# Kernel optimization log

Measured on AMD Instinct MI355X. Metric: run time of the kernel, lower is better.

The kernel has to match this reference:

```python
import jax, jax.numpy as jnp
import numpy as np

B, L, D, H = 2, 2048, 1024, 16
HD = D // H
SCALE = 1.0 / (HD ** 0.5)


def setup_inputs() -> dict:
    key = jax.random.key(0)
    ks = jax.random.split(key, 8)
    s = 0.02  # keep pre-softmax logits in a sane range
    return {
        "x": jax.random.normal(ks[0], (B, L, D), dtype=jnp.float32),
        "attn_biases": jax.random.normal(ks[1], (B, H, L, L), dtype=jnp.float32) * 0.1,
        "attn_mask": jnp.zeros((B, 1, L, L), dtype=jnp.float32),
        "Wq": jax.random.normal(ks[2], (D, D), dtype=jnp.float32) * s,
        "bq": jnp.zeros((D,), dtype=jnp.float32),
        "Wk": jax.random.normal(ks[3], (D, D), dtype=jnp.float32) * s,
        "bk": jnp.zeros((D,), dtype=jnp.float32),
        "Wv": jax.random.normal(ks[4], (D, D), dtype=jnp.float32) * s,
        "bv": jnp.zeros((D,), dtype=jnp.float32),
        "Wo": jax.random.normal(ks[5], (D, D), dtype=jnp.float32) * s,
        "bo": jnp.zeros((D,), dtype=jnp.float32),
    }


def reference(x, attn_biases, attn_mask, Wq, bq, Wk, bk, Wv, bv, Wo, bo):
    b, l, d = x.shape
    # torch nn.Linear: y = x @ W.T + b
    q = (x @ Wq.T + bq).reshape(b, l, H, HD)
    k = (x @ Wk.T + bk).reshape(b, l, H, HD)
    v = (x @ Wv.T + bv).reshape(b, l, H, HD)
    # scores: (B, H, Lq, Lk)
    scores = SCALE * jnp.einsum("bqhd,bkhd->bhqk", q, k)
    scores = scores + attn_biases + attn_mask
    probs = jax.nn.softmax(scores, axis=-1)
    out = jnp.einsum("bhqk,bkhd->bqhd", probs, v).reshape(b, l, d)
    return out @ Wo.T + bo
```

## Files before the change

### kernel.cpp

```cpp
#include <hip/hip_runtime.h>
#include <stdint.h>

#define SCALE_ 0.125f

typedef unsigned short u16;
typedef __attribute__((ext_vector_type(8))) __bf16 bf16x8;
typedef __attribute__((ext_vector_type(4))) float f32x4;
typedef __attribute__((ext_vector_type(4))) unsigned int u32x4;

__device__ __forceinline__ void gload16(const void* g, void* l) {
  __builtin_amdgcn_global_load_lds(
      (const __attribute__((address_space(1))) unsigned int*)g,
      (__attribute__((address_space(3))) unsigned int*)l, 16, 0, 0);
}

__device__ __forceinline__ u16 f2bf(float f) {
  union { float f; unsigned int u; } v; v.f = f;
  return (u16)((v.u + 0x7FFFu + ((v.u >> 16) & 1u)) >> 16);
}

__device__ __forceinline__ bf16x8 ld_bf8(const u16* p) {
  return *reinterpret_cast<const bf16x8*>(p);
}

__global__ __launch_bounds__(256) void cvt_kernel(
    const float* __restrict__ x, const float* __restrict__ wq,
    const float* __restrict__ wk, const float* __restrict__ wv,
    const float* __restrict__ wo, u16* __restrict__ ws) {
  long e0 = ((long)blockIdx.x * 256 + threadIdx.x) * 8;
  const float* src; u16* dst; long off;
  if (e0 < 4194304L) {
    src = x; dst = ws; off = e0;
  } else {
    long tt = e0 - 4194304L;
    int w = (int)(tt >> 20);
    off = tt & 1048575L;
    src = (w == 0) ? wq : (w == 1) ? wk : (w == 2) ? wv : wo;
    dst = ws + 4194304L + (long)w * 1048576L;
  }
  float4 f0 = *(const float4*)(src + off);
  float4 f1 = *(const float4*)(src + off + 4);
  union { u16 u[8]; u32x4 v; } r;
  r.u[0] = f2bf(f0.x); r.u[1] = f2bf(f0.y); r.u[2] = f2bf(f0.z); r.u[3] = f2bf(f0.w);
  r.u[4] = f2bf(f1.x); r.u[5] = f2bf(f1.y); r.u[6] = f2bf(f1.z); r.u[7] = f2bf(f1.w);
  *reinterpret_cast<u32x4*>(dst + off) = r.v;
}

__global__ __launch_bounds__(256) void gemm_bt(
    const u16* __restrict__ A,
    const u16* __restrict__ W0, const u16* __restrict__ W1, const u16* __restrict__ W2,
    const float* __restrict__ b0, const float* __restrict__ b1, const float* __restrict__ b2,
    void* __restrict__ d0, void* __restrict__ d1, void* __restrict__ d2,
    int mode_base) {
  __shared__ u16 lsA[128 * 32];
  __shared__ u16 lsB[128 * 32];

  const int z = blockIdx.z;
  const int mode = mode_base + z;
  const u16* W = (z == 0) ? W0 : (z == 1) ? W1 : W2;
  const float* bias = (z == 0) ? b0 : (z == 1) ? b1 : b2;
  void* dst = (z == 0) ? d0 : (z == 1) ? d1 : d2;
  const float scale = (mode == 0) ? SCALE_ : 1.0f;

  const int t = threadIdx.x;
  const int bm = blockIdx.y, bn = blockIdx.x;
  const int lane = t & 63, lr = lane & 15, lg = lane >> 4;
  const int wid = t >> 6, wr = wid >> 1, wc = wid & 1;

  f32x4 zero = {0.f, 0.f, 0.f, 0.f};
  f32x4 acc[4][4];
#pragma unroll
  for (int i = 0; i < 4; ++i)
#pragma unroll
    for (int j = 0; j < 4; ++j) acc[i][j] = zero;

  const u16* gA = A + (size_t)(bm * 128) * 1024;
  const u16* gB = W + (size_t)(bn * 128) * 1024;
  const int srow = t >> 2, scol = (t & 3) * 8;

  for (int kt = 0; kt < 32; ++kt) {
    const int k0 = kt * 32;
    __syncthreads();
    gload16(gA + (size_t)srow * 1024 + k0 + scol,        &lsA[t * 8]);
    gload16(gA + (size_t)(srow + 64) * 1024 + k0 + scol, &lsA[2048 + t * 8]);
    gload16(gB + (size_t)srow * 1024 + k0 + scol,        &lsB[t * 8]);
    gload16(gB + (size_t)(srow + 64) * 1024 + k0 + scol, &lsB[2048 + t * 8]);
    __syncthreads();

    bf16x8 af[4], bf[4];
#pragma unroll
    for (int mi = 0; mi < 4; ++mi)
      af[mi] = ld_bf8(&lsA[(wr * 64 + mi * 16 + lr) * 32 + lg * 8]);
#pragma unroll
    for (int ni = 0; ni < 4; ++ni)
      bf[ni] = ld_bf8(&lsB[(wc * 64 + ni * 16 + lr) * 32 + lg * 8]);
#pragma unroll
    for (int mi = 0; mi < 4; ++mi)
#pragma unroll
      for (int ni = 0; ni < 4; ++ni)
        acc[mi][ni] = __builtin_amdgcn_mfma_f32_16x16x32_bf16(af[mi], bf[ni], acc[mi][ni], 0, 0, 0);
  }

#pragma unroll
  for (int ni = 0; ni < 4; ++ni) {
    const int gcol = bn * 128 + wc * 64 + ni * 16 + lr;
    const float bv = bias[gcol];
#pragma unroll
    for (int mi = 0; mi < 4; ++mi) {
      const int growb = bm * 128 + wr * 64 + mi * 16 + lg * 4;
#pragma unroll
      for (int j = 0; j < 4; ++j) {
        const int grow = growb + j;
        const float val = (acc[mi][ni][j] + bv) * scale;
        if (mode == 3) {
          ((float*)dst)[(size_t)grow * 1024 + gcol] = val;
        } else {
          const int b = grow >> 11, l = grow & 2047, h = gcol >> 6, hd = gcol & 63;
          size_t idx;
          if (mode == 2) idx = (((size_t)(b * 16 + h)) * 64 + hd) * 2048 + l;
          else           idx = (((size_t)(b * 16 + h)) * 2048 + l) * 64 + hd;
          ((u16*)dst)[idx] = f2bf(val);
        }
      }
    }
  }
}

__global__ __launch_bounds__(256) void gemm_out64(
    const u16* __restrict__ A, const u16* __restrict__ W,
    const float* __restrict__ bias, float* __restrict__ out) {
  __shared__ u16 lsA[64 * 32];
  __shared__ u16 lsB[128 * 32];

  const int t = threadIdx.x;
  const int bm = blockIdx.y, bn = blockIdx.x;
  const int lane = t & 63, lr = lane & 15, lg = lane >> 4;
  const int wid = t >> 6;

  f32x4 zero = {0.f, 0.f, 0.f, 0.f};
  f32x4 acc[4][2];
#pragma unroll
  for (int i = 0; i < 4; ++i) { acc[i][0] = zero; acc[i][1] = zero; }

  const u16* gA = A + (size_t)(bm * 64) * 1024;
  const u16* gB = W + (size_t)(bn * 128) * 1024;
  const int srow = t >> 2, scol = (t & 3) * 8;

  for (int kt = 0; kt < 32; ++kt) {
    const int k0 = kt * 32;
    __syncthreads();
    gload16(gA + (size_t)srow * 1024 + k0 + scol,        &lsA[t * 8]);
    gload16(gB + (size_t)srow * 1024 + k0 + scol,        &lsB[t * 8]);
    gload16(gB + (size_t)(srow + 64) * 1024 + k0 + scol, &lsB[2048 + t * 8]);
    __syncthreads();

    bf16x8 af[4], bf[2];
#pragma unroll
    for (int mi = 0; mi < 4; ++mi)
      af[mi] = ld_bf8(&lsA[(mi * 16 + lr) * 32 + lg * 8]);
#pragma unroll
    for (int ni = 0; ni < 2; ++ni)
      bf[ni] = ld_bf8(&lsB[(wid * 32 + ni * 16 + lr) * 32 + lg * 8]);
#pragma unroll
    for (int mi = 0; mi < 4; ++mi)
#pragma unroll
      for (int ni = 0; ni < 2; ++ni)
        acc[mi][ni] = __builtin_amdgcn_mfma_f32_16x16x32_bf16(af[mi], bf[ni], acc[mi][ni], 0, 0, 0);
  }

#pragma unroll
  for (int ni = 0; ni < 2; ++ni) {
    const int gcol = bn * 128 + wid * 32 + ni * 16 + lr;
    const float bv = bias[gcol];
#pragma unroll
    for (int mi = 0; mi < 4; ++mi) {
      const int growb = bm * 64 + mi * 16 + lg * 4;
#pragma unroll
      for (int j = 0; j < 4; ++j)
        out[(size_t)(growb + j) * 1024 + gcol] = acc[mi][ni][j] + bv;
    }
  }
}

__global__ __launch_bounds__(256, 4) void attn_kernel(
    const u16* __restrict__ Q, const u16* __restrict__ Kb_, const u16* __restrict__ Vtb,
    const float* __restrict__ bias, const float* __restrict__ mask,
    u16* __restrict__ attn) {
  __shared__ u16 lsK[64 * 64];
  __shared__ u16 lsV[64 * 64];
  __shared__ u16 lsP[4][16 * 88];

  const int t = threadIdx.x, wid = t >> 6, lane = t & 63, lr = lane & 15, lg = lane >> 4;
  const int q0 = blockIdx.x * 64;
  const int h = blockIdx.y, b = blockIdx.z;
  const int bh = b * 16 + h;

  const u16* qb = Q + ((size_t)bh * 2048 + q0 + wid * 16) * 64;
  const u16* kb = Kb_ + (size_t)bh * 2048 * 64;
  const u16* vb = Vtb + (size_t)bh * 64 * 2048;
  const float* biasr = bias + (size_t)bh * 2048 * 2048;
  const float* maskr = mask + (size_t)b * 2048 * 2048;

  bf16x8 qf[2];
  qf[0] = ld_bf8(qb + (size_t)lr * 64 + lg * 8);
  qf[1] = ld_bf8(qb + (size_t)lr * 64 + 32 + lg * 8);

  float lsum[4] = {0.f, 0.f, 0.f, 0.f};
  f32x4 zero = {0.f, 0.f, 0.f, 0.f};
  f32x4 o[4];
#pragma unroll
  for (int i = 0; i < 4; ++i) o[i] = zero;

  const int srow = t >> 3;
  const int swz = ((t & 7) ^ (srow & 7)) * 8;
  const int rsw = (lr & 7) * 8;
  const int qrow0 = q0 + wid * 16 + lg * 4;

  for (int kt = 0; kt < 32; ++kt) {
    const int k0 = kt * 64;

    float bb[4][4];
#pragma unroll
    for (int j = 0; j < 4; ++j) {
      const float* br = biasr + (size_t)(qrow0 + j) * 2048 + k0 + lr;
      const float* mr = maskr + (size_t)(qrow0 + j) * 2048 + k0 + lr;
#pragma unroll
      for (int n = 0; n < 4; ++n) bb[j][n] = br[n * 16] + mr[n * 16];
    }

    __syncthreads();
    gload16(kb + (size_t)(k0 + srow) * 64 + swz,        &lsK[t * 8]);
    gload16(kb + (size_t)(k0 + srow + 32) * 64 + swz,   &lsK[2048 + t * 8]);
    gload16(vb + (size_t)srow * 2048 + k0 + swz,        &lsV[t * 8]);
    gload16(vb + (size_t)(srow + 32) * 2048 + k0 + swz, &lsV[2048 + t * 8]);
    __syncthreads();

    f32x4 s[4];
#pragma unroll
    for (int n = 0; n < 4; ++n) s[n] = zero;
#pragma unroll
    for (int ks = 0; ks < 2; ++ks)
#pragma unroll
      for (int n = 0; n < 4; ++n) {
        bf16x8 kf = ld_bf8(&lsK[((n * 16 + lr) * 64 + ks * 32 + lg * 8) ^ rsw]);
        s[n] = __builtin_amdgcn_mfma_f32_16x16x32_bf16(qf[ks], kf, s[n], 0, 0, 0);
      }

#pragma unroll
    for (int i = 0; i < 4; ++i) {
      float rs = 0.f;
#pragma unroll
      for (int n = 0; n < 4; ++n) {
        float p = __expf(s[n][i] + bb[i][n]);
        s[n][i] = p;
        rs += p;
      }
      lsum[i] += rs;
    }

#pragma unroll
    for (int n = 0; n < 4; ++n)
#pragma unroll
      for (int i = 0; i < 4; ++i)
        lsP[wid][(lg * 4 + i) * 88 + n * 16 + lr] = f2bf(s[n][i]);
    asm volatile("s_waitcnt lgkmcnt(0)" ::: "memory");
    __builtin_amdgcn_sched_barrier(0);

#pragma unroll
    for (int ks = 0; ks < 2; ++ks) {
      bf16x8 pa = ld_bf8(&lsP[wid][lr * 88 + ks * 32 + lg * 8]);
#pragma unroll
      for (int dt = 0; dt < 4; ++dt) {
        bf16x8 vf = ld_bf8(&lsV[((dt * 16 + lr) * 64 + ks * 32 + lg * 8) ^ rsw]);
        o[dt] = __builtin_amdgcn_mfma_f32_16x16x32_bf16(pa, vf, o[dt], 0, 0, 0);
      }
    }
  }

#pragma unroll
  for (int i = 0; i < 4; ++i) {
    lsum[i] += __shfl_xor(lsum[i], 1);
    lsum[i] += __shfl_xor(lsum[i], 2);
    lsum[i] += __shfl_xor(lsum[i], 4);
    lsum[i] += __shfl_xor(lsum[i], 8);
  }
  float inv[4];
#pragma unroll
  for (int i = 0; i < 4; ++i) inv[i] = 1.0f / lsum[i];
#pragma unroll
  for (int dt = 0; dt < 4; ++dt) {
    const int dcol = h * 64 + dt * 16 + lr;
#pragma unroll
    for (int i = 0; i < 4; ++i)
      attn[((size_t)b * 2048 + qrow0 + i) * 1024 + dcol] = f2bf(o[dt][i] * inv[i]);
  }
}

extern "C" void kernel_launch(void* const* d_in, const int* in_sizes, int n_in,
                              void* d_out, int out_size, void* d_ws, size_t ws_size,
                              hipStream_t stream) {
  const float* x    = (const float*)d_in[0];
  const float* bias = (const float*)d_in[1];
  const float* mask = (const float*)d_in[2];
  const float* Wq   = (const float*)d_in[3];
  const float* bq   = (const float*)d_in[4];
  const float* Wk   = (const float*)d_in[5];
  const float* bk   = (const float*)d_in[6];
  const float* Wv   = (const float*)d_in[7];
  const float* bv   = (const float*)d_in[8];
  const float* Wo   = (const float*)d_in[9];
  const float* bo   = (const float*)d_in[10];
  float* out = (float*)d_out;

  u16* ws   = (u16*)d_ws;
  u16* xb   = ws;
  u16* wqb  = ws + 4194304L;
  u16* wkb  = wqb + 1048576L;
  u16* wvb  = wkb + 1048576L;
  u16* wob  = wvb + 1048576L;
  u16* Qb   = wob + 1048576L;
  u16* Kb   = Qb + 4194304L;
  u16* Vtb  = Kb + 4194304L;
  u16* attnb = Vtb + 4194304L;

  cvt_kernel<<<4096, 256, 0, stream>>>(x, Wq, Wk, Wv, Wo, ws);

  dim3 gqkv(8, 32, 3);
  gemm_bt<<<gqkv, 256, 0, stream>>>(xb, wqb, wkb, wvb, bq, bk, bv,
                                    (void*)Qb, (void*)Kb, (void*)Vtb, 0);

  attn_kernel<<<dim3(32, 16, 2), 256, 0, stream>>>(Qb, Kb, Vtb, bias, mask, attnb);

  gemm_out64<<<dim3(8, 64), 256, 0, stream>>>(attnb, wob, bo, out);
}
```

Baseline: 241.3 us.

## Double-buffer K/V tiles, prefetch bias, and use exp2 with 512-thread attention blocks

The attention kernel now runs 512 threads per block covering 128 query rows, so each K/V tile in LDS is shared by eight waves. K/V tiles are double-buffered, with the next tile's loads issued before the current tile's compute, which leaves one barrier per iteration. The next tile's bias and mask are loaded after QK^T. Q is pre-scaled by scale·log2e and bias is multiplied by log2e, so softmax uses exp2 and the bias seeds the MFMA accumulator. LDS use per block roughly doubles, and occupancy under launch_bounds(512,4) may change.

```diff
diff --git a/kernel.cpp b/kernel.cpp
--- a/kernel.cpp
+++ b/kernel.cpp
@@ -1,7 +1,8 @@
 #include <hip/hip_runtime.h>
 #include <stdint.h>
 
-#define SCALE_ 0.125f
+#define QSCALE_ 0.18033688f
+#define LOG2E_  1.44269504f
 
 typedef unsigned short u16;
 typedef __attribute__((ext_vector_type(8))) __bf16 bf16x8;
@@ -60,7 +61,7 @@
   const u16* W = (z == 0) ? W0 : (z == 1) ? W1 : W2;
   const float* bias = (z == 0) ? b0 : (z == 1) ? b1 : b2;
   void* dst = (z == 0) ? d0 : (z == 1) ? d1 : d2;
-  const float scale = (mode == 0) ? SCALE_ : 1.0f;
+  const float scale = (mode == 0) ? QSCALE_ : 1.0f;
 
   const int t = threadIdx.x;
   const int bm = blockIdx.y, bn = blockIdx.x;
@@ -182,16 +183,18 @@
   }
 }
 
-__global__ __launch_bounds__(256, 4) void attn_kernel(
+__global__ __launch_bounds__(512, 4) void attn_kernel(
     const u16* __restrict__ Q, const u16* __restrict__ Kb_, const u16* __restrict__ Vtb,
     const float* __restrict__ bias, const float* __restrict__ mask,
     u16* __restrict__ attn) {
-  __shared__ u16 lsK[64 * 64];
-  __shared__ u16 lsV[64 * 64];
-  __shared__ u16 lsP[4][16 * 88];
+  __shared__ u16 lsK0[64 * 64];
+  __shared__ u16 lsK1[64 * 64];
+  __shared__ u16 lsV0[64 * 64];
+  __shared__ u16 lsV1[64 * 64];
+  __shared__ u16 lsP[8][16 * 88];
 
   const int t = threadIdx.x, wid = t >> 6, lane = t & 63, lr = lane & 15, lg = lane >> 4;
-  const int q0 = blockIdx.x * 64;
+  const int q0 = blockIdx.x * 128;
   const int h = blockIdx.y, b = blockIdx.z;
   const int bh = b * 16 + h;
 
@@ -206,56 +209,56 @@
   qf[1] = ld_bf8(qb + (size_t)lr * 64 + 32 + lg * 8);
 
   float lsum[4] = {0.f, 0.f, 0.f, 0.f};
-  f32x4 zero = {0.f, 0.f, 0.f, 0.f};
   f32x4 o[4];
 #pragma unroll
-  for (int i = 0; i < 4; ++i) o[i] = zero;
+  for (int i = 0; i < 4; ++i) o[i] = (f32x4){0.f, 0.f, 0.f, 0.f};
 
   const int srow = t >> 3;
   const int swz = ((t & 7) ^ (srow & 7)) * 8;
   const int rsw = (lr & 7) * 8;
   const int qrow0 = q0 + wid * 16 + lg * 4;
 
-  for (int kt = 0; kt < 32; ++kt) {
+  float bb[4][4];
+  auto bbload = [&](int kt_) __attribute__((always_inline)) {
+    const int kk = kt_ * 64;
+#pragma unroll
+    for (int j = 0; j < 4; ++j) {
+      const float* br = biasr + (size_t)(qrow0 + j) * 2048 + kk + lr;
+      const float* mr = maskr + (size_t)(qrow0 + j) * 2048 + kk + lr;
+#pragma unroll
+      for (int n = 0; n < 4; ++n) bb[j][n] = (br[n * 16] + mr[n * 16]) * LOG2E_;
+    }
+  };
+
+  auto iter = [&](u16* lsKc, u16* lsVc, u16* lsKn, u16* lsVn, int kt)
+      __attribute__((always_inline)) {
     const int k0 = kt * 64;
-
-    float bb[4][4];
-#pragma unroll
-    for (int j = 0; j < 4; ++j) {
-      const float* br = biasr + (size_t)(qrow0 + j) * 2048 + k0 + lr;
-      const float* mr = maskr + (size_t)(qrow0 + j) * 2048 + k0 + lr;
-#pragma unroll
-      for (int n = 0; n < 4; ++n) bb[j][n] = br[n * 16] + mr[n * 16];
-    }
-
-    __syncthreads();
-    gload16(kb + (size_t)(k0 + srow) * 64 + swz,        &lsK[t * 8]);
-    gload16(kb + (size_t)(k0 + srow + 32) * 64 + swz,   &lsK[2048 + t * 8]);
-    gload16(vb + (size_t)srow * 2048 + k0 + swz,        &lsV[t * 8]);
-    gload16(vb + (size_t)(srow + 32) * 2048 + k0 + swz, &lsV[2048 + t * 8]);
-    __syncthreads();
+    if (kt < 31) {
+      const int kk = k0 + 64;
+      gload16(kb + (size_t)(kk + srow) * 64 + swz, &lsKn[t * 8]);
+      gload16(vb + (size_t)srow * 2048 + kk + swz, &lsVn[t * 8]);
+    }
 
     f32x4 s[4];
 #pragma unroll
-    for (int n = 0; n < 4; ++n) s[n] = zero;
+    for (int n = 0; n < 4; ++n)
+      s[n] = (f32x4){bb[0][n], bb[1][n], bb[2][n], bb[3][n]};
 #pragma unroll
     for (int ks = 0; ks < 2; ++ks)
 #pragma unroll
       for (int n = 0; n < 4; ++n) {
-        bf16x8 kf = ld_bf8(&lsK[((n * 16 + lr) * 64 + ks * 32 + lg * 8) ^ rsw]);
+        bf16x8 kf = ld_bf8(&lsKc[((n * 16 + lr) * 64 + ks * 32 + lg * 8) ^ rsw]);
         s[n] = __builtin_amdgcn_mfma_f32_16x16x32_bf16(qf[ks], kf, s[n], 0, 0, 0);
       }
 
+    bbload(kt < 31 ? kt + 1 : 31);
+
 #pragma unroll
     for (int i = 0; i < 4; ++i) {
-      float rs = 0.f;
-#pragma unroll
-      for (int n = 0; n < 4; ++n) {
-        float p = __expf(s[n][i] + bb[i][n]);
-        s[n][i] = p;
-        rs += p;
-      }
-      lsum[i] += rs;
+      float p0 = exp2f(s[0][i]), p1 = exp2f(s[1][i]);
+      float p2 = exp2f(s[2][i]), p3 = exp2f(s[3][i]);
+      s[0][i] = p0; s[1][i] = p1; s[2][i] = p2; s[3][i] = p3;
+      lsum[i] += (p0 + p1) + (p2 + p3);
     }
 
 #pragma unroll
@@ -271,10 +274,22 @@
       bf16x8 pa = ld_bf8(&lsP[wid][lr * 88 + ks * 32 + lg * 8]);
 #pragma unroll
       for (int dt = 0; dt < 4; ++dt) {
-        bf16x8 vf = ld_bf8(&lsV[((dt * 16 + lr) * 64 + ks * 32 + lg * 8) ^ rsw]);
+        bf16x8 vf = ld_bf8(&lsVc[((dt * 16 + lr) * 64 + ks * 32 + lg * 8) ^ rsw]);
         o[dt] = __builtin_amdgcn_mfma_f32_16x16x32_bf16(pa, vf, o[dt], 0, 0, 0);
       }
     }
+
+    __syncthreads();
+  };
+
+  gload16(kb + (size_t)srow * 64 + swz, &lsK0[t * 8]);
+  gload16(vb + (size_t)srow * 2048 + swz, &lsV0[t * 8]);
+  bbload(0);
+  __syncthreads();
+
+  for (int kt = 0; kt < 32; kt += 2) {
+    iter(lsK0, lsV0, lsK1, lsV1, kt);
+    iter(lsK1, lsV1, lsK0, lsV0, kt + 1);
   }
 
 #pragma unroll
@@ -329,7 +344,7 @@
   gemm_bt<<<gqkv, 256, 0, stream>>>(xb, wqb, wkb, wvb, bq, bk, bv,
                                     (void*)Qb, (void*)Kb, (void*)Vtb, 0);
 
-  attn_kernel<<<dim3(32, 16, 2), 256, 0, stream>>>(Qb, Kb, Vtb, bias, mask, attnb);
+  attn_kernel<<<dim3(16, 16, 2), 512, 0, stream>>>(Qb, Kb, Vtb, bias, mask, attnb);
 
   gemm_out64<<<dim3(8, 64), 256, 0, stream>>>(attnb, wob, bo, out);
 }
```

Result: slower. 370.2 us (+53.4%).

## Transpose QK MFMA so bias loads vectorize and use exp2 with folded log2e

Applied to the files above, without the earlier changes.

The QK^T MFMA now takes its operands in swapped order, so each lane holds four consecutive key columns of a single query row. This lets the bias and mask be read as contiguous float4 loads instead of 16 scattered scalar loads per tile, and lets P be written to LDS as packed 8-byte stores. The log2(e) factor is folded into the Q scale in the projection GEMM and into the bias, so exp2f replaces __expf. The row-sum reduction becomes one accumulator reduced across lane groups, then redistributed with a shuffle. Bias loads are the dominant HBM traffic (about 537 MB of fp32), so coalescing them is the main goal.

```diff
diff --git a/kernel.cpp b/kernel.cpp
--- a/kernel.cpp
+++ b/kernel.cpp
@@ -1,12 +1,14 @@
 #include <hip/hip_runtime.h>
 #include <stdint.h>
 
-#define SCALE_ 0.125f
+#define QSCALE_ 0.18033688f
+#define LOG2E_  1.44269504f
 
 typedef unsigned short u16;
 typedef __attribute__((ext_vector_type(8))) __bf16 bf16x8;
 typedef __attribute__((ext_vector_type(4))) float f32x4;
 typedef __attribute__((ext_vector_type(4))) unsigned int u32x4;
+typedef __attribute__((ext_vector_type(2))) unsigned int u32x2;
 
 __device__ __forceinline__ void gload16(const void* g, void* l) {
   __builtin_amdgcn_global_load_lds(
@@ -60,7 +62,7 @@
   const u16* W = (z == 0) ? W0 : (z == 1) ? W1 : W2;
   const float* bias = (z == 0) ? b0 : (z == 1) ? b1 : b2;
   void* dst = (z == 0) ? d0 : (z == 1) ? d1 : d2;
-  const float scale = (mode == 0) ? SCALE_ : 1.0f;
+  const float scale = (mode == 0) ? QSCALE_ : 1.0f;
 
   const int t = threadIdx.x;
   const int bm = blockIdx.y, bn = blockIdx.x;
@@ -198,18 +200,18 @@
   const u16* qb = Q + ((size_t)bh * 2048 + q0 + wid * 16) * 64;
   const u16* kb = Kb_ + (size_t)bh * 2048 * 64;
   const u16* vb = Vtb + (size_t)bh * 64 * 2048;
-  const float* biasr = bias + (size_t)bh * 2048 * 2048;
-  const float* maskr = mask + (size_t)b * 2048 * 2048;
+  const int qlr = q0 + wid * 16 + lr;
+  const float* biasq = bias + (size_t)bh * 2048 * 2048 + (size_t)qlr * 2048;
+  const float* maskq = mask + (size_t)b * 2048 * 2048 + (size_t)qlr * 2048;
 
   bf16x8 qf[2];
   qf[0] = ld_bf8(qb + (size_t)lr * 64 + lg * 8);
   qf[1] = ld_bf8(qb + (size_t)lr * 64 + 32 + lg * 8);
 
-  float lsum[4] = {0.f, 0.f, 0.f, 0.f};
-  f32x4 zero = {0.f, 0.f, 0.f, 0.f};
+  float lsum = 0.f;
   f32x4 o[4];
 #pragma unroll
-  for (int i = 0; i < 4; ++i) o[i] = zero;
+  for (int i = 0; i < 4; ++i) o[i] = (f32x4){0.f, 0.f, 0.f, 0.f};
 
   const int srow = t >> 3;
   const int swz = ((t & 7) ^ (srow & 7)) * 8;
@@ -219,13 +221,12 @@
   for (int kt = 0; kt < 32; ++kt) {
     const int k0 = kt * 64;
 
-    float bb[4][4];
-#pragma unroll
-    for (int j = 0; j < 4; ++j) {
-      const float* br = biasr + (size_t)(qrow0 + j) * 2048 + k0 + lr;
-      const float* mr = maskr + (size_t)(qrow0 + j) * 2048 + k0 + lr;
-#pragma unroll
-      for (int n = 0; n < 4; ++n) bb[j][n] = br[n * 16] + mr[n * 16];
+    f32x4 bb[4];
+#pragma unroll
+    for (int n = 0; n < 4; ++n) {
+      f32x4 b4 = *(const f32x4*)(biasq + k0 + n * 16 + lg * 4);
+      f32x4 m4 = *(const f32x4*)(maskq + k0 + n * 16 + lg * 4);
+      bb[n] = (b4 + m4) * LOG2E_;
     }
 
     __syncthreads();
@@ -237,32 +238,31 @@
 
     f32x4 s[4];
 #pragma unroll
-    for (int n = 0; n < 4; ++n) s[n] = zero;
+    for (int n = 0; n < 4; ++n) s[n] = (f32x4){0.f, 0.f, 0.f, 0.f};
 #pragma unroll
     for (int ks = 0; ks < 2; ++ks)
 #pragma unroll
       for (int n = 0; n < 4; ++n) {
         bf16x8 kf = ld_bf8(&lsK[((n * 16 + lr) * 64 + ks * 32 + lg * 8) ^ rsw]);
-        s[n] = __builtin_amdgcn_mfma_f32_16x16x32_bf16(qf[ks], kf, s[n], 0, 0, 0);
+        s[n] = __builtin_amdgcn_mfma_f32_16x16x32_bf16(kf, qf[ks], s[n], 0, 0, 0);
       }
 
 #pragma unroll
-    for (int i = 0; i < 4; ++i) {
-      float rs = 0.f;
-#pragma unroll
-      for (int n = 0; n < 4; ++n) {
-        float p = __expf(s[n][i] + bb[i][n]);
-        s[n][i] = p;
-        rs += p;
-      }
-      lsum[i] += rs;
-    }
-
-#pragma unroll
-    for (int n = 0; n < 4; ++n)
-#pragma unroll
-      for (int i = 0; i < 4; ++i)
-        lsP[wid][(lg * 4 + i) * 88 + n * 16 + lr] = f2bf(s[n][i]);
+    for (int n = 0; n < 4; ++n) {
+      s[n] += bb[n];
+      float p0 = exp2f(s[n][0]), p1 = exp2f(s[n][1]);
+      float p2 = exp2f(s[n][2]), p3 = exp2f(s[n][3]);
+      s[n][0] = p0; s[n][1] = p1; s[n][2] = p2; s[n][3] = p3;
+      lsum += (p0 + p1) + (p2 + p3);
+    }
+
+#pragma unroll
+    for (int n = 0; n < 4; ++n) {
+      unsigned int lo = (unsigned int)f2bf(s[n][0]) | ((unsigned int)f2bf(s[n][1]) << 16);
+      unsigned int hi = (unsigned int)f2bf(s[n][2]) | ((unsigned int)f2bf(s[n][3]) << 16);
+      u32x2 w = {lo, hi};
+      *(u32x2*)&lsP[wid][lr * 88 + n * 16 + lg * 4] = w;
+    }
     asm volatile("s_waitcnt lgkmcnt(0)" ::: "memory");
     __builtin_amdgcn_sched_barrier(0);
 
@@ -277,16 +277,11 @@
     }
   }
 
-#pragma unroll
-  for (int i = 0; i < 4; ++i) {
-    lsum[i] += __shfl_xor(lsum[i], 1);
-    lsum[i] += __shfl_xor(lsum[i], 2);
-    lsum[i] += __shfl_xor(lsum[i], 4);
-    lsum[i] += __shfl_xor(lsum[i], 8);
-  }
+  lsum += __shfl_xor(lsum, 16);
+  lsum += __shfl_xor(lsum, 32);
   float inv[4];
 #pragma unroll
-  for (int i = 0; i < 4; ++i) inv[i] = 1.0f / lsum[i];
+  for (int i = 0; i < 4; ++i) inv[i] = 1.0f / __shfl(lsum, lg * 4 + i);
 #pragma unroll
   for (int dt = 0; dt < 4; ++dt) {
     const int dcol = h * 64 + dt * 16 + lr;
```

Measured after the change: 266.6 us. +10.5%, slower.
